# Optimization experiments

Measured on AMD Instinct MI355X. Metric: run time of the kernel, lower is better.

## Reference

```python
import jax, jax.numpy as jnp
import numpy as np

V = 32000; D = 512; H = 8; DH = D // H; L = 12; E = 8; FF = 2048
B = 2; S = 1024; MAXPOS = 2048
EPS = 1e-6; NEG = -1e9


def _rmsnorm(x, w):
    return x * jax.lax.rsqrt(jnp.mean(x * x, axis=-1, keepdims=True) + EPS) * w


def setup_inputs() -> dict:
    key = jax.random.key(0)
    ks = jax.random.split(key, 10)
    s = 0.02
    n = lambda k, shp: jax.random.normal(k, shp, jnp.float32) * s
    return {
        "input_ids": jax.random.randint(ks[0], (B, S), 0, V),
        "tok_emb": n(ks[1], (V, D)),
        "pos_emb": n(ks[2], (MAXPOS, D)),
        "Wqkv": n(ks[3], (L, D, 3 * D)), "bqkv": jnp.zeros((L, 3 * D), jnp.float32),
        "Wo": n(ks[4], (L, D, D)), "bo": jnp.zeros((L, D), jnp.float32),
        "rW": n(ks[5], (L, D, E)), "rb": jnp.zeros((L, E), jnp.float32),
        "eW1": n(ks[6], (L, E, D, FF)), "eb1": jnp.zeros((L, E, FF), jnp.float32),
        "eW2": n(ks[7], (L, E, FF, D)), "eb2": jnp.zeros((L, E, D), jnp.float32),
        "n1w": jnp.ones((L, D), jnp.float32), "n2w": jnp.ones((L, D), jnp.float32),
        "now": jnp.ones((D,), jnp.float32), "lmW": n(ks[8], (D, V)),
    }


def _forward(input_ids, tok_emb, pos_emb, Wqkv, bqkv, Wo, bo, rW, rb,
             eW1, eb1, eW2, eb2, n1w, n2w, now, lmW):
    x = tok_emb[input_ids] + pos_emb[:S]              # [B,S,D]
    causal = jnp.tril(jnp.ones((S, S), bool))         # lower-triangular mask

    def step(x, p):
        wqkv, bq, wo, bo_, rw, rb_, w1, b1, w2, b2, g1, g2 = p
        # --- causal self-attention ---
        h = _rmsnorm(x, g1)
        qkv = h @ wqkv + bq
        q, k, v = [t.reshape(B, S, H, DH) for t in jnp.split(qkv, 3, axis=-1)]
        scores = jnp.einsum('bqhd,bkhd->bhqk', q, k) / jnp.sqrt(jnp.float32(DH))
        scores = jnp.where(causal, scores, NEG)
        attn = jax.nn.softmax(scores, axis=-1)
        o = jnp.einsum('bhqk,bkhd->bqhd', attn, v).reshape(B, S, D) @ wo + bo_
        x = x + o
        # --- MoE layer, top-1 routing ---
        h = _rmsnorm(x, g2)
        rl = h @ rw + rb_                              # router logits [B,S,E]
        probs = jax.nn.softmax(rl, axis=-1)
        top_w = jnp.max(probs, axis=-1)                # top-1 gate weight [B,S]
        top_i = jnp.argmax(probs, axis=-1)             # expert id [B,S]
        one_hot = jax.nn.one_hot(top_i, E, dtype=x.dtype)
        frac = jnp.mean(one_hot, axis=(0, 1))          # fraction of tokens per expert
        pmean = jnp.mean(probs, axis=(0, 1))           # mean router prob per expert
        aux = E * jnp.sum(frac * pmean)                # switch-style load-balance loss
        disp = (one_hot * top_w[..., None]).reshape(-1, E)   # [T,E] weighted dispatch
        hf = h.reshape(-1, D)                          # [T,D]
        hid = jax.nn.gelu(jnp.einsum('td,edf->etf', hf, w1) + b1[:, None, :], approximate=False)
        outs = jnp.einsum('etf,efd->etd', hid, w2) + b2[:, None, :]
        y = jnp.einsum('etd,te->td', outs, disp).reshape(B, S, D)  # scatter-combine
        x = x + y
        return x, (aux, rl)

    x, (auxes, rlogits) = jax.lax.scan(
        step, x, (Wqkv, bqkv, Wo, bo, rW, rb, eW1, eb1, eW2, eb2, n1w, n2w))
    logits = _rmsnorm(x, now) @ lmW                    # [B,S,V]
    return logits, jnp.sum(auxes), rlogits


def reference(input_ids, tok_emb, pos_emb, Wqkv, bqkv, Wo, bo, rW, rb,
              eW1, eb1, eW2, eb2, n1w, n2w, now, lmW):
    return _forward(input_ids, tok_emb, pos_emb, Wqkv, bqkv, Wo, bo, rW, rb,
                    eW1, eb1, eW2, eb2, n1w, n2w, now, lmW)
```

## Files before the change

kernel.cpp:

```cpp
#include <hip/hip_runtime.h>

constexpr int B_  = 2, S_ = 1024, T_ = 2048;
constexpr int D_  = 512, H_ = 8, DH_ = 64;
constexpr int L_  = 12, E_ = 8, FF_ = 2048;
constexpr int V_  = 32000, D3_ = 1536;

using half8_t = __attribute__((ext_vector_type(8))) _Float16;
using half2_t = __attribute__((ext_vector_type(2))) _Float16;
using f32x4_t = __attribute__((ext_vector_type(4))) float;

__device__ __forceinline__ float wred(float v){
#pragma unroll
  for (int off = 32; off; off >>= 1) v += __shfl_xor(v, off);
  return v;
}
__device__ __forceinline__ float gelu_f(float v){
  return 0.5f * v * (1.f + erff(v * 0.70710678118654752f));
}

__global__ void k_embed(const int* __restrict__ ids, const float* __restrict__ tok,
                        const float* __restrict__ pos, float* __restrict__ x){
  int t = blockIdx.x;
  int s = t & (S_ - 1);
  int id = ids[t];
  const float* tr = tok + (size_t)id * D_;
  const float* pr = pos + (size_t)s  * D_;
  float* xr = x + (size_t)t * D_;
  for (int d = threadIdx.x; d < D_; d += blockDim.x) xr[d] = tr[d] + pr[d];
}

__global__ __launch_bounds__(64) void k_norm_router(
    const float* __restrict__ x, const float* __restrict__ nw,
    const float* __restrict__ rW, const float* __restrict__ rb,
    float* __restrict__ h, float* __restrict__ rl_out,
    float* __restrict__ topw, int* __restrict__ topi){
  const int t = blockIdx.x, lane = threadIdx.x;
  const float* xr = x + (size_t)t * D_;
  const float4 xv0 = *reinterpret_cast<const float4*>(xr + (lane << 2));
  const float4 xv1 = *reinterpret_cast<const float4*>(xr + 256 + (lane << 2));
  float ss = xv0.x*xv0.x + xv0.y*xv0.y + xv0.z*xv0.z + xv0.w*xv0.w
           + xv1.x*xv1.x + xv1.y*xv1.y + xv1.z*xv1.z + xv1.w*xv1.w;
  ss = wred(ss);
  const float sc = rsqrtf(ss * (1.f / (float)D_) + 1e-6f);
  const float4 w0 = *reinterpret_cast<const float4*>(nw + (lane << 2));
  const float4 w1 = *reinterpret_cast<const float4*>(nw + 256 + (lane << 2));
  float hv[8];
  hv[0] = xv0.x*sc*w0.x; hv[1] = xv0.y*sc*w0.y; hv[2] = xv0.z*sc*w0.z; hv[3] = xv0.w*sc*w0.w;
  hv[4] = xv1.x*sc*w1.x; hv[5] = xv1.y*sc*w1.y; hv[6] = xv1.z*sc*w1.z; hv[7] = xv1.w*sc*w1.w;
  float* hr = h + (size_t)t * D_;
  *reinterpret_cast<float4*>(hr + (lane << 2))       = make_float4(hv[0], hv[1], hv[2], hv[3]);
  *reinterpret_cast<float4*>(hr + 256 + (lane << 2)) = make_float4(hv[4], hv[5], hv[6], hv[7]);
  float acc[8] = {0,0,0,0,0,0,0,0};
#pragma unroll
  for (int u = 0; u < 8; u++){
    const int d = (u < 4) ? ((lane << 2) + u) : (256 + (lane << 2) + u - 4);
    const float4 ra = *reinterpret_cast<const float4*>(rW + (size_t)d * E_);
    const float4 rb4 = *reinterpret_cast<const float4*>(rW + (size_t)d * E_ + 4);
    acc[0] += hv[u]*ra.x;  acc[1] += hv[u]*ra.y;  acc[2] += hv[u]*ra.z;  acc[3] += hv[u]*ra.w;
    acc[4] += hv[u]*rb4.x; acc[5] += hv[u]*rb4.y; acc[6] += hv[u]*rb4.z; acc[7] += hv[u]*rb4.w;
  }
  float rl[8];
#pragma unroll
  for (int e = 0; e < 8; e++) rl[e] = wred(acc[e]) + rb[e];
  float mx = rl[0];
#pragma unroll
  for (int e = 1; e < 8; e++) mx = fmaxf(mx, rl[e]);
  float p[8], s = 0.f;
#pragma unroll
  for (int e = 0; e < 8; e++){ p[e] = __expf(rl[e] - mx); s += p[e]; }
  const float inv = 1.f / s;
  int arg = 0; float best = rl[0];
#pragma unroll
  for (int e = 1; e < 8; e++) if (rl[e] > best){ best = rl[e]; arg = e; }
  if (lane == 0){
#pragma unroll
    for (int e = 0; e < 8; e++) rl_out[(size_t)t * E_ + e] = rl[e];
    topw[t] = p[arg] * inv;
    topi[t] = arg;
  }
}

__global__ __launch_bounds__(1024) void k_route_scan2(
    const int* __restrict__ topi, const float* __restrict__ rl,
    int* __restrict__ seg, int* __restrict__ perm, float* __restrict__ aux){
  __shared__ int cnt[8], segs[9], cur[8];
  __shared__ float psums[8];
  const int tid = threadIdx.x;
  if (tid < 8){ cnt[tid] = 0; psums[tid] = 0.f; }
  __syncthreads();
  const int t0 = tid, t1 = tid + 1024;
  const int e0 = topi[t0], e1 = topi[t1];
  atomicAdd(&cnt[e0], 1);
  atomicAdd(&cnt[e1], 1);
  float ps[8] = {0,0,0,0,0,0,0,0};
#pragma unroll
  for (int k = 0; k < 2; k++){
    const float* r = rl + (size_t)(k ? t1 : t0) * E_;
    float v[8];
#pragma unroll
    for (int e = 0; e < 8; e++) v[e] = r[e];
    float mx = v[0];
#pragma unroll
    for (int e = 1; e < 8; e++) mx = fmaxf(mx, v[e]);
    float s = 0.f;
#pragma unroll
    for (int e = 0; e < 8; e++){ v[e] = __expf(v[e] - mx); s += v[e]; }
    const float is = 1.f / s;
#pragma unroll
    for (int e = 0; e < 8; e++) ps[e] += v[e] * is;
  }
#pragma unroll
  for (int e = 0; e < 8; e++) ps[e] = wred(ps[e]);
  if ((tid & 63) == 0){
#pragma unroll
    for (int e = 0; e < 8; e++) atomicAdd(&psums[e], ps[e]);
  }
  __syncthreads();
  if (tid == 0){
    segs[0] = 0;
#pragma unroll
    for (int e = 0; e < 8; e++) segs[e + 1] = segs[e] + cnt[e];
#pragma unroll
    for (int e = 0; e < 8; e++) cur[e] = segs[e];
  }
  __syncthreads();
  if (tid < 9) seg[tid] = segs[tid];
  const int p0 = atomicAdd(&cur[e0], 1); perm[p0] = t0;
  const int p1 = atomicAdd(&cur[e1], 1); perm[p1] = t1;
  if (tid == 0){
    float av = 0.f;
#pragma unroll
    for (int e = 0; e < 8; e++) av += (float)cnt[e] * psums[e];
    aux[0] += 8.f * av * (1.f / ((float)T_ * (float)T_));
  }
}

template<int BM, int BN, int NPROD, int EPI, bool MOE, bool APERM, int SWZROWS, bool ANORM>
__global__ __launch_bounds__(256) void k_mgemm(
    const float* __restrict__ A, const float* __restrict__ Bm,
    const float* __restrict__ bias, float* __restrict__ C,
    int M, int N, int K,
    const int* __restrict__ seg, const int* __restrict__ perm,
    const float* __restrict__ topw, const float* __restrict__ nw){
  constexpr int FM = BM / 32, FN = BN / 32;
  constexpr int BSLOTS = BN / 64;
  const int tid = threadIdx.x;
  int rowTile, colTile;
  if (SWZROWS > 0){
    const int nwg = gridDim.x;
    const int bid = blockIdx.x;
    const int lb = (bid & 7) * (nwg >> 3) + (bid >> 3);
    rowTile = lb % SWZROWS;
    colTile = lb / SWZROWS;
  } else {
    colTile = blockIdx.x; rowTile = blockIdx.y;
  }
  int e = 0, s0 = 0, cnt = M;
  if (MOE){ e = blockIdx.z; s0 = seg[e]; cnt = seg[e + 1] - s0; }
  const int row0 = rowTile * BM, col0 = colTile * BN;
  if (MOE && row0 >= cnt) return;
  const float* Bp = Bm + (size_t)e * K * N;
  const float* bp = bias + (size_t)e * N;

  __shared__ __align__(16) _Float16 Ah[BM * 32];
  __shared__ __align__(16) _Float16 Al[NPROD == 3 ? BM * 32 : 8];
  __shared__ __align__(16) _Float16 Bh[BN * 32];
  __shared__ __align__(16) _Float16 Bl[NPROD == 3 ? BN * 32 : 8];

  const int am = (BM == 64) ? (tid >> 2) : (tid >> 1);
  const int agrow = row0 + am;
  const bool aval = agrow < cnt;
  const float* Arow = nullptr;
  if (aval){
    int ridx = APERM ? perm[s0 + agrow] : (MOE ? s0 + agrow : agrow);
    Arow = A + (size_t)ridx * K;
  }
  const int asub = am >> 4;

  const int lane = tid & 63, w = tid >> 6;
  const int wm0 = (w >> 1) * (BM / 2), wn0 = (w & 1) * (BN / 2);

  float ascale = 1.f;
  if (ANORM){
    float ss = 0.f;
    if (BM == 64){
      const int kg = tid & 3;
      for (int k0 = 0; k0 < K; k0 += 32){
        const float4 a0 = *reinterpret_cast<const float4*>(Arow + k0 + (kg << 3));
        const float4 a1 = *reinterpret_cast<const float4*>(Arow + k0 + (kg << 3) + 4);
        ss += a0.x*a0.x + a0.y*a0.y + a0.z*a0.z + a0.w*a0.w
            + a1.x*a1.x + a1.y*a1.y + a1.z*a1.z + a1.w*a1.w;
      }
      ss += __shfl_xor(ss, 1);
      ss += __shfl_xor(ss, 2);
    } else {
      const int kgb = (tid & 1) << 1;
      for (int k0 = 0; k0 < K; k0 += 32){
#pragma unroll
        for (int kq = 0; kq < 2; kq++){
          const int kg = kgb + kq;
          const float4 a0 = *reinterpret_cast<const float4*>(Arow + k0 + (kg << 3));
          const float4 a1 = *reinterpret_cast<const float4*>(Arow + k0 + (kg << 3) + 4);
          ss += a0.x*a0.x + a0.y*a0.y + a0.z*a0.z + a0.w*a0.w
              + a1.x*a1.x + a1.y*a1.y + a1.z*a1.z + a1.w*a1.w;
        }
      }
      ss += __shfl_xor(ss, 1);
    }
    ascale = rsqrtf(ss * (1.f / (float)K) + 1e-6f);
  }

  f32x4_t acc_hh[FM][FN];
  f32x4_t acc_mx[NPROD == 3 ? FM : 1][NPROD == 3 ? FN : 1];
#pragma unroll
  for (int i = 0; i < FM; i++)
#pragma unroll
    for (int j = 0; j < FN; j++){
      acc_hh[i][j] = (f32x4_t){0.f, 0.f, 0.f, 0.f};
      if (NPROD == 3) acc_mx[i][j] = (f32x4_t){0.f, 0.f, 0.f, 0.f};
    }

  for (int k0 = 0; k0 < K; k0 += 32){
    if (BM == 64){
      const int kg = tid & 3;
      float4 av0 = make_float4(0,0,0,0), av1 = make_float4(0,0,0,0);
      if (aval){
        av0 = *reinterpret_cast<const float4*>(Arow + k0 + (kg << 3));
        av1 = *reinterpret_cast<const float4*>(Arow + k0 + (kg << 3) + 4);
      }
      float a8[8] = {av0.x, av0.y, av0.z, av0.w, av1.x, av1.y, av1.z, av1.w};
      if (ANORM){
        const float4 w0 = *reinterpret_cast<const float4*>(nw + k0 + (kg << 3));
        const float4 w1 = *reinterpret_cast<const float4*>(nw + k0 + (kg << 3) + 4);
        const float wn8[8] = {w0.x, w0.y, w0.z, w0.w, w1.x, w1.y, w1.z, w1.w};
#pragma unroll
        for (int u = 0; u < 8; u++) a8[u] *= ascale * wn8[u];
      }
      half8_t hi, lo;
#pragma unroll
      for (int u = 0; u < 8; u++){
        hi[u] = (_Float16)a8[u];
        if (NPROD == 3) lo[u] = (_Float16)((a8[u] - (float)hi[u]) * 2048.f);
      }
      const int lidx = (am & 15) + (kg << 4);
      const int base = asub * 512 + ((lidx ^ (asub & 7)) << 3);
      *reinterpret_cast<half8_t*>(&Ah[base]) = hi;
      if (NPROD == 3) *reinterpret_cast<half8_t*>(&Al[base]) = lo;
    } else {
      const int kgb = (tid & 1) << 1;
#pragma unroll
      for (int kq = 0; kq < 2; kq++){
        const int kg = kgb + kq;
        float4 av0 = make_float4(0,0,0,0), av1 = make_float4(0,0,0,0);
        if (aval){
          av0 = *reinterpret_cast<const float4*>(Arow + k0 + (kg << 3));
          av1 = *reinterpret_cast<const float4*>(Arow + k0 + (kg << 3) + 4);
        }
        float a8[8] = {av0.x, av0.y, av0.z, av0.w, av1.x, av1.y, av1.z, av1.w};
        if (ANORM){
          const float4 w0 = *reinterpret_cast<const float4*>(nw + k0 + (kg << 3));
          const float4 w1 = *reinterpret_cast<const float4*>(nw + k0 + (kg << 3) + 4);
          const float wn8[8] = {w0.x, w0.y, w0.z, w0.w, w1.x, w1.y, w1.z, w1.w};
#pragma unroll
          for (int u = 0; u < 8; u++) a8[u] *= ascale * wn8[u];
        }
        half8_t hi;
#pragma unroll
        for (int u = 0; u < 8; u++) hi[u] = (_Float16)a8[u];
        const int lidx = (am & 15) + (kg << 4);
        *reinterpret_cast<half8_t*>(&Ah[asub * 512 + ((lidx ^ (asub & 7)) << 3)]) = hi;
      }
    }
#pragma unroll
    for (int sl = 0; sl < BSLOTS; sl++){
      const int sid = sl * 256 + tid;
      const int col = sid & (BN - 1);
      const int kg  = sid / BN;
      const float* bpp = Bp + (size_t)(k0 + (kg << 3)) * N + col0 + col;
      half8_t hi, lo;
#pragma unroll
      for (int ee = 0; ee < 8; ee++){
        const float v = bpp[(size_t)ee * N];
        hi[ee] = (_Float16)v;
        if (NPROD == 3) lo[ee] = (_Float16)((v - (float)hi[ee]) * 2048.f);
      }
      const int sub = col >> 4;
      const int lidx = (col & 15) + (kg << 4);
      const int base = sub * 512 + ((lidx ^ (sub & 7)) << 3);
      *reinterpret_cast<half8_t*>(&Bh[base]) = hi;
      if (NPROD == 3) *reinterpret_cast<half8_t*>(&Bl[base]) = lo;
    }
    __syncthreads();
    half8_t fAh[FM], fBh[FN];
    half8_t fAl[NPROD == 3 ? FM : 1], fBl[NPROD == 3 ? FN : 1];
#pragma unroll
    for (int fm = 0; fm < FM; fm++){
      const int s = (wm0 >> 4) + fm;
      const int ofs = s * 512 + ((lane ^ (s & 7)) << 3);
      fAh[fm] = *reinterpret_cast<const half8_t*>(&Ah[ofs]);
      if (NPROD == 3) fAl[fm] = *reinterpret_cast<const half8_t*>(&Al[ofs]);
    }
#pragma unroll
    for (int fn = 0; fn < FN; fn++){
      const int s = (wn0 >> 4) + fn;
      const int ofs = s * 512 + ((lane ^ (s & 7)) << 3);
      fBh[fn] = *reinterpret_cast<const half8_t*>(&Bh[ofs]);
      if (NPROD == 3) fBl[fn] = *reinterpret_cast<const half8_t*>(&Bl[ofs]);
    }
#pragma unroll
    for (int fm = 0; fm < FM; fm++)
#pragma unroll
      for (int fn = 0; fn < FN; fn++){
        acc_hh[fm][fn] = __builtin_amdgcn_mfma_f32_16x16x32_f16(
            fAh[fm], fBh[fn], acc_hh[fm][fn], 0, 0, 0);
        if (NPROD == 3){
          acc_mx[fm][fn] = __builtin_amdgcn_mfma_f32_16x16x32_f16(
              fAh[fm], fBl[fn], acc_mx[fm][fn], 0, 0, 0);
          acc_mx[fm][fn] = __builtin_amdgcn_mfma_f32_16x16x32_f16(
              fAl[fm], fBh[fn], acc_mx[fm][fn], 0, 0, 0);
        }
      }
    __syncthreads();
  }

  const int lr = lane & 15, kg4 = lane >> 4;
#pragma unroll
  for (int fm = 0; fm < FM; fm++){
#pragma unroll
    for (int reg = 0; reg < 4; reg++){
      const int grow = row0 + wm0 + fm * 16 + (kg4 << 2) + reg;
      if (grow >= cnt) continue;
      int trow = 0; float tw = 0.f;
      if (EPI == 3){ trow = perm[s0 + grow]; tw = topw[trow]; }
#pragma unroll
      for (int fn = 0; fn < FN; fn++){
        const int col = col0 + wn0 + fn * 16 + lr;
        float v = acc_hh[fm][fn][reg];
        if (NPROD == 3) v += acc_mx[fm][fn][reg] * (1.f / 2048.f);
        if (EPI == 0){
          C[(size_t)grow * N + col] = v + bp[col];
        } else if (EPI == 1){
          C[(size_t)grow * N + col] += v + bp[col];
        } else if (EPI == 2){
          C[(size_t)(s0 + grow) * N + col] = gelu_f(v + bp[col]);
        } else if (EPI == 3){
          C[(size_t)trow * N + col] += tw * (v + bp[col]);
        } else {
          C[(size_t)grow * N + col] = v;
        }
      }
    }
  }
}

__global__ __launch_bounds__(256) void k_attn5(const float* __restrict__ qkv,
                                               float* __restrict__ o,
                                               float* __restrict__ attp,
                                               float* __restrict__ attml){
  __shared__ __align__(16) _Float16 Khi[4096], Klo[4096], Vhi[4096], Vlo[4096];
  __shared__ __align__(16) float pbuf[4][16 * 68];
  const int tid = threadIdx.x, w = tid >> 6, lane = tid & 63;
  const int lr = lane & 15, g = lane >> 4;
  const int bid = blockIdx.x;
  int bh, qt, kt0, kt1, mode;
  if (bid < 128){        bh = bid >> 3;            qt = 8 + (bid & 7);  kt0 = 0; kt1 = 7;  mode = 1; }
  else if (bid < 256){   const int j = bid - 128;  bh = j >> 3; qt = 7 - (j & 7);  kt0 = 0; kt1 = qt; mode = 0; }
  else {                 const int j = bid - 256;  bh = j >> 3; qt = 15 - (j & 7); kt0 = 8; kt1 = qt; mode = 2; }
  const int b = bh >> 3, h = bh & 7;
  const size_t bbase = (size_t)(b << 10) * D3_;
  const int hoff = h * 64;
  const int qg = (qt << 6) + (w << 4) + lr;

  half8_t qhi[2], qlo[2];
#pragma unroll
  for (int ks = 0; ks < 2; ks++){
    const float* qp = qkv + bbase + (size_t)qg * D3_ + hoff + ks * 32 + g * 8;
    const float4 f0 = *reinterpret_cast<const float4*>(qp);
    const float4 f1 = *reinterpret_cast<const float4*>(qp + 4);
    const float qa[8] = {f0.x, f0.y, f0.z, f0.w, f1.x, f1.y, f1.z, f1.w};
#pragma unroll
    for (int e = 0; e < 8; e++){
      const float v = qa[e] * 0.125f;
      const _Float16 hi = (_Float16)v;
      qhi[ks][e] = hi;
      qlo[ks][e] = (_Float16)((v - (float)hi) * 2048.f);
    }
  }

  float m = -1e30f, l = 0.f;
  f32x4_t oacc[4];
#pragma unroll
  for (int s = 0; s < 4; s++) oacc[s] = (f32x4_t){0.f, 0.f, 0.f, 0.f};

  const int kK = tid >> 2, quad = tid & 3;
  const int kp = tid >> 3, oct = tid & 7;

  float ka[16], va[8], vb[8];
  auto loadregs = [&](int kt){
    const int j0 = kt << 6;
    const float* kr = qkv + bbase + (size_t)(j0 + kK) * D3_ + 512 + hoff + quad * 16;
    const float4 f0 = *reinterpret_cast<const float4*>(kr);
    const float4 f1 = *reinterpret_cast<const float4*>(kr + 4);
    const float4 f2 = *reinterpret_cast<const float4*>(kr + 8);
    const float4 f3 = *reinterpret_cast<const float4*>(kr + 12);
    ka[0]=f0.x; ka[1]=f0.y; ka[2]=f0.z; ka[3]=f0.w;
    ka[4]=f1.x; ka[5]=f1.y; ka[6]=f1.z; ka[7]=f1.w;
    ka[8]=f2.x; ka[9]=f2.y; ka[10]=f2.z; ka[11]=f2.w;
    ka[12]=f3.x; ka[13]=f3.y; ka[14]=f3.z; ka[15]=f3.w;
    const int k0v = kp << 1;
    const float* vr = qkv + bbase + (size_t)(j0 + k0v) * D3_ + 1024 + hoff + oct * 8;
    const float4 a0 = *reinterpret_cast<const float4*>(vr);
    const float4 a1 = *reinterpret_cast<const float4*>(vr + 4);
    const float4 b0 = *reinterpret_cast<const float4*>(vr + D3_);
    const float4 b1 = *reinterpret_cast<const float4*>(vr + D3_ + 4);
    va[0]=a0.x; va[1]=a0.y; va[2]=a0.z; va[3]=a0.w;
    va[4]=a1.x; va[5]=a1.y; va[6]=a1.z; va[7]=a1.w;
    vb[0]=b0.x; vb[1]=b0.y; vb[2]=b0.z; vb[3]=b0.w;
    vb[4]=b1.x; vb[5]=b1.y; vb[6]=b1.z; vb[7]=b1.w;
  };
  auto writelds = [&](){
    const int ksd = quad >> 1;
#pragma unroll
    for (int ch = 0; ch < 2; ch++){
      const int kgd = ((quad << 1) + ch) & 3;
      const int base = ksd * 2048 + (kK >> 4) * 512 + (((kK & 15) + (kgd << 4)) << 3);
      half8_t hi, lo;
#pragma unroll
      for (int e = 0; e < 8; e++){
        const float v = ka[ch * 8 + e];
        const _Float16 hv = (_Float16)v;
        hi[e] = hv;
        lo[e] = (_Float16)((v - (float)hv) * 2048.f);
      }
      *reinterpret_cast<half8_t*>(&Khi[base]) = hi;
      *reinterpret_cast<half8_t*>(&Klo[base]) = lo;
    }
    const int ksk = kp >> 4, kgk = (kp >> 2) & 3, e0 = (kp & 3) << 1;
#pragma unroll
    for (int j = 0; j < 8; j++){
      const int d = oct * 8 + j;
      const int lidx = (d & 15) + (kgk << 4);
      const int sw = lidx ^ kgk ^ (ksk << 2);
      const int fa = ksk * 2048 + (d >> 4) * 512 + (sw << 3) + e0;
      const _Float16 h0 = (_Float16)va[j], h1 = (_Float16)vb[j];
      *reinterpret_cast<half2_t*>(&Vhi[fa]) = (half2_t){h0, h1};
      const _Float16 l0 = (_Float16)((va[j] - (float)h0) * 2048.f);
      const _Float16 l1 = (_Float16)((vb[j] - (float)h1) * 2048.f);
      *reinterpret_cast<half2_t*>(&Vlo[fa]) = (half2_t){l0, l1};
    }
  };

  loadregs(kt0);
  for (int kt = kt0; kt <= kt1; kt++){
    const int j0 = kt << 6;
    __syncthreads();
    writelds();
    if (kt < kt1) loadregs(kt + 1);
    __syncthreads();

    f32x4_t dfr[4];
#pragma unroll
    for (int s = 0; s < 4; s++){
      f32x4_t acc = (f32x4_t){0.f, 0.f, 0.f, 0.f};
      f32x4_t mix = (f32x4_t){0.f, 0.f, 0.f, 0.f};
#pragma unroll
      for (int ks = 0; ks < 2; ks++){
        const int base = ks * 2048 + s * 512 + lane * 8;
        const half8_t khi = *reinterpret_cast<const half8_t*>(&Khi[base]);
        const half8_t klo = *reinterpret_cast<const half8_t*>(&Klo[base]);
        acc = __builtin_amdgcn_mfma_f32_16x16x32_f16(khi, qhi[ks], acc, 0, 0, 0);
        mix = __builtin_amdgcn_mfma_f32_16x16x32_f16(khi, qlo[ks], mix, 0, 0, 0);
        mix = __builtin_amdgcn_mfma_f32_16x16x32_f16(klo, qhi[ks], mix, 0, 0, 0);
      }
#pragma unroll
      for (int r = 0; r < 4; r++) dfr[s][r] = acc[r] + mix[r] * (1.f / 2048.f);
    }
    if (kt == qt){
#pragma unroll
      for (int s = 0; s < 4; s++)
#pragma unroll
        for (int r = 0; r < 4; r++){
          const int keyg = j0 + (g << 2) + r + (s << 4);
          if (keyg > qg) dfr[s][r] = -1e30f;
        }
    }
    float mloc = dfr[0][0];
#pragma unroll
    for (int s = 0; s < 4; s++)
#pragma unroll
      for (int r = 0; r < 4; r++) mloc = fmaxf(mloc, dfr[s][r]);
    mloc = fmaxf(mloc, __shfl_xor(mloc, 16));
    mloc = fmaxf(mloc, __shfl_xor(mloc, 32));
    const float mn = fmaxf(m, mloc);
    const float cr = __expf(m - mn);
    float psum = 0.f;
#pragma unroll
    for (int s = 0; s < 4; s++)
#pragma unroll
      for (int r = 0; r < 4; r++){
        const float p = __expf(dfr[s][r] - mn);
        psum += p;
        pbuf[w][lr * 68 + (s << 4) + (g << 2) + r] = p;
      }
    psum += __shfl_xor(psum, 16);
    psum += __shfl_xor(psum, 32);
    l = l * cr + psum;
    m = mn;
#pragma unroll
    for (int s = 0; s < 4; s++)
#pragma unroll
      for (int r = 0; r < 4; r++) oacc[s][r] *= cr;

    half8_t phi[2], plo[2];
#pragma unroll
    for (int ks = 0; ks < 2; ks++){
      const float* pp = &pbuf[w][lr * 68 + ks * 32 + g * 8];
      const float4 p0 = *reinterpret_cast<const float4*>(pp);
      const float4 p1 = *reinterpret_cast<const float4*>(pp + 4);
      const float pa[8] = {p0.x,p0.y,p0.z,p0.w, p1.x,p1.y,p1.z,p1.w};
#pragma unroll
      for (int e = 0; e < 8; e++){
        const _Float16 hv = (_Float16)pa[e];
        phi[ks][e] = hv;
        plo[ks][e] = (_Float16)((pa[e] - (float)hv) * 2048.f);
      }
    }
#pragma unroll
    for (int s = 0; s < 4; s++){
      f32x4_t mix = (f32x4_t){0.f, 0.f, 0.f, 0.f};
#pragma unroll
      for (int ks = 0; ks < 2; ks++){
        const int sw = lane ^ g ^ (ks << 2);
        const int base = ks * 2048 + s * 512 + sw * 8;
        const half8_t vhi = *reinterpret_cast<const half8_t*>(&Vhi[base]);
        const half8_t vlo = *reinterpret_cast<const half8_t*>(&Vlo[base]);
        oacc[s] = __builtin_amdgcn_mfma_f32_16x16x32_f16(vhi, phi[ks], oacc[s], 0, 0, 0);
        mix = __builtin_amdgcn_mfma_f32_16x16x32_f16(vhi, plo[ks], mix, 0, 0, 0);
        mix = __builtin_amdgcn_mfma_f32_16x16x32_f16(vlo, phi[ks], mix, 0, 0, 0);
      }
#pragma unroll
      for (int r = 0; r < 4; r++) oacc[s][r] += mix[r] * (1.f / 2048.f);
    }
  }

  if (mode == 0){
    const float linv = 1.f / l;
    float* orow = o + (size_t)((b << 10) + qg) * D_ + hoff;
#pragma unroll
    for (int s = 0; s < 4; s++)
#pragma unroll
      for (int r = 0; r < 4; r++){
        const int d = (g << 2) + r + (s << 4);
        orow[d] = oacc[s][r] * linv;
      }
  } else {
    const int pidx = (((bh << 3) + (qt - 8)) << 1) + (mode - 1);
    float* pO = attp + (size_t)pidx * 4096;
    const int qloc = (w << 4) + lr;
#pragma unroll
    for (int s = 0; s < 4; s++)
#pragma unroll
      for (int r = 0; r < 4; r++){
        const int d = (g << 2) + r + (s << 4);
        pO[qloc * 64 + d] = oacc[s][r];
      }
    if (g == 0){
      attml[pidx * 128 + qloc]      = m;
      attml[pidx * 128 + 64 + qloc] = l;
    }
  }
}

__global__ __launch_bounds__(256) void k_attn_comb(const float* __restrict__ attp,
                                                   const float* __restrict__ attml,
                                                   float* __restrict__ o){
  const int bid = blockIdx.x;
  const int bh = bid >> 3, i = bid & 7, qt = 8 + i;
  const int b = bh >> 3, h = bh & 7;
  const int pidx0 = ((bh << 3) + i) << 1;
  const float* pA = attp + (size_t)pidx0 * 4096;
  const float* pB = pA + 4096;
  const float* mlA = attml + pidx0 * 128;
  const float* mlB = mlA + 128;
  const int tid = threadIdx.x;
  const int q = tid >> 2, dg = (tid & 3) << 4;
  const float mA = mlA[q], lA = mlA[64 + q];
  const float mB = mlB[q], lB = mlB[64 + q];
  const float M = fmaxf(mA, mB);
  const float cA = __expf(mA - M), cB = __expf(mB - M);
  const float linv = 1.f / (lA * cA + lB * cB);
  float* orow = o + (size_t)((b << 10) + (qt << 6) + q) * D_ + h * 64;
#pragma unroll
  for (int j = 0; j < 4; j++){
    const int d = dg + (j << 2);
    const float4 a = *reinterpret_cast<const float4*>(pA + q * 64 + d);
    const float4 bb = *reinterpret_cast<const float4*>(pB + q * 64 + d);
    *reinterpret_cast<float4*>(orow + d) = make_float4(
        (a.x * cA + bb.x * cB) * linv, (a.y * cA + bb.y * cB) * linv,
        (a.z * cA + bb.z * cB) * linv, (a.w * cA + bb.w * cB) * linv);
  }
}

extern "C" void kernel_launch(void* const* d_in, const int* in_sizes, int n_in,
                              void* d_out, int out_size, void* d_ws, size_t ws_size,
                              hipStream_t stream){
  const int*   ids  = (const int*)  d_in[0];
  const float* tok  = (const float*)d_in[1];
  const float* pos  = (const float*)d_in[2];
  const float* Wqkv = (const float*)d_in[3];
  const float* bqkv = (const float*)d_in[4];
  const float* Wo   = (const float*)d_in[5];
  const float* bo   = (const float*)d_in[6];
  const float* rW   = (const float*)d_in[7];
  const float* rb   = (const float*)d_in[8];
  const float* eW1  = (const float*)d_in[9];
  const float* eb1  = (const float*)d_in[10];
  const float* eW2  = (const float*)d_in[11];
  const float* eb2  = (const float*)d_in[12];
  const float* n1w  = (const float*)d_in[13];
  const float* n2w  = (const float*)d_in[14];
  const float* noww = (const float*)d_in[15];
  const float* lmW  = (const float*)d_in[16];

  float* out    = (float*)d_out;
  float* logits = out;
  float* aux    = out + (size_t)T_ * V_;
  float* rlog   = aux + 1;

  float* ws = (float*)d_ws;
  size_t off = 0;
  float* x     = ws + off; off += (size_t)T_ * D_;
  float* h     = ws + off; off += (size_t)T_ * D_;
  float* qkv   = ws + off; off += (size_t)T_ * D3_;
  float* attno = ws + off; off += (size_t)T_ * D_;
  float* hid   = ws + off; off += (size_t)T_ * FF_;
  float* topw  = ws + off; off += T_;
  int* topi    = (int*)(ws + off); off += T_;
  int* perm    = (int*)(ws + off); off += T_;
  int* seg     = (int*)(ws + off); off += (E_ + 1);
  float* attp  = ws + off; off += 16 * 8 * 2 * 4096;
  float* attml = ws + off; off += 16 * 8 * 2 * 128;

  hipMemsetAsync(aux, 0, sizeof(float), stream);
  k_embed<<<T_, 256, 0, stream>>>(ids, tok, pos, x);

  for (int l = 0; l < L_; l++){
    k_mgemm<64, 128, 3, 0, false, false, 0, true><<<dim3(D3_ / 128, T_ / 64), 256, 0, stream>>>(
        x, Wqkv + (size_t)l * D_ * D3_, bqkv + (size_t)l * D3_, qkv,
        T_, D3_, D_, seg, perm, topw, n1w + (size_t)l * D_);
    k_attn5<<<384, 256, 0, stream>>>(qkv, attno, attp, attml);
    k_attn_comb<<<128, 256, 0, stream>>>(attp, attml, attno);
    k_mgemm<64, 64, 3, 1, false, false, 0, false><<<dim3(D_ / 64, T_ / 64), 256, 0, stream>>>(
        attno, Wo + (size_t)l * D_ * D_, bo + (size_t)l * D_, x,
        T_, D_, D_, seg, perm, topw, nullptr);
    k_norm_router<<<T_, 64, 0, stream>>>(x, n2w + (size_t)l * D_,
        rW + (size_t)l * D_ * E_, rb + (size_t)l * E_,
        h, rlog + (size_t)l * T_ * E_, topw, topi);
    k_route_scan2<<<1, 1024, 0, stream>>>(topi, rlog + (size_t)l * T_ * E_, seg, perm, aux);
    k_mgemm<64, 128, 3, 2, true, true, 0, false><<<dim3(FF_ / 128, T_ / 64, E_), 256, 0, stream>>>(
        h, eW1 + (size_t)l * E_ * D_ * FF_, eb1 + (size_t)l * E_ * FF_, hid,
        T_, FF_, D_, seg, perm, topw, nullptr);
    k_mgemm<64, 64, 3, 3, true, false, 0, false><<<dim3(D_ / 64, T_ / 64, E_), 256, 0, stream>>>(
        hid, eW2 + (size_t)l * E_ * FF_ * D_, eb2 + (size_t)l * E_ * D_, x,
        T_, D_, FF_, seg, perm, topw, nullptr);
  }

  k_mgemm<128, 128, 1, 4, false, false, 16, true><<<(T_ / 128) * (V_ / 128), 256, 0, stream>>>(
      x, lmW, nullptr, logits, T_, V_, D_, seg, perm, topw, noww);
}
```

Measured before the change: 3.214 ms.

## Prefetch next K-tile into registers and pre-pack LM head weights to fp16

The GEMM main loop now loads the next K-step's A and B tiles into registers before the MFMA work on the current tile, then writes them to shared memory after the barrier. This is register-level software pipelining meant to hide global-load latency behind compute. A new prep kernel converts the LM-head weight matrix to fp16 in the exact swizzled tile layout, so the vocab GEMM can do contiguous half8 copies instead of strided fp32 loads plus conversion. The packed weights reuse the qkv/attno/hid workspace. The costs are an extra full pass over lmW on every call and higher register pressure from the prefetch buffers.

```diff
diff --git a/kernel.cpp b/kernel.cpp
--- a/kernel.cpp
+++ b/kernel.cpp
@@ -135,13 +135,29 @@
   }
 }
 
-template<int BM, int BN, int NPROD, int EPI, bool MOE, bool APERM, int SWZROWS, bool ANORM>
+__global__ __launch_bounds__(256) void k_prep_lm(const float* __restrict__ Bsrc,
+                                                 _Float16* __restrict__ Bpre){
+  const int gid = blockIdx.x * 256 + threadIdx.x;
+  const int n = gid % V_;
+  const int kb = gid / V_;
+  const int kstep = kb >> 2, kg = kb & 3;
+  const int colTile = n >> 7, nl = n & 127;
+  const int sub = nl >> 4;
+  const int lsw = ((nl & 15) + (kg << 4)) ^ (sub & 7);
+  half8_t v;
+#pragma unroll
+  for (int e = 0; e < 8; e++) v[e] = (_Float16)Bsrc[(size_t)(kb * 8 + e) * V_ + n];
+  *reinterpret_cast<half8_t*>(&Bpre[(((size_t)colTile * 16 + kstep) << 12) + sub * 512 + lsw * 8]) = v;
+}
+
+template<int BM, int BN, int NPROD, int EPI, bool MOE, bool APERM, int SWZROWS, bool ANORM, bool BPRE>
 __global__ __launch_bounds__(256) void k_mgemm(
     const float* __restrict__ A, const float* __restrict__ Bm,
     const float* __restrict__ bias, float* __restrict__ C,
     int M, int N, int K,
     const int* __restrict__ seg, const int* __restrict__ perm,
-    const float* __restrict__ topw, const float* __restrict__ nw){
+    const float* __restrict__ topw, const float* __restrict__ nw,
+    const _Float16* __restrict__ Bpre){
   constexpr int FM = BM / 32, FN = BN / 32;
   constexpr int BSLOTS = BN / 64;
   const int tid = threadIdx.x;
@@ -210,25 +226,54 @@
     ascale = rsqrtf(ss * (1.f / (float)K) + 1e-6f);
   }
 
-  f32x4_t acc_hh[FM][FN];
-  f32x4_t acc_mx[NPROD == 3 ? FM : 1][NPROD == 3 ? FN : 1];
-#pragma unroll
-  for (int i = 0; i < FM; i++)
-#pragma unroll
-    for (int j = 0; j < FN; j++){
-      acc_hh[i][j] = (f32x4_t){0.f, 0.f, 0.f, 0.f};
-      if (NPROD == 3) acc_mx[i][j] = (f32x4_t){0.f, 0.f, 0.f, 0.f};
-    }
-
-  for (int k0 = 0; k0 < K; k0 += 32){
-    if (BM == 64){
-      const int kg = tid & 3;
-      float4 av0 = make_float4(0,0,0,0), av1 = make_float4(0,0,0,0);
+  float areg[(BM == 64) ? 8 : 1];
+  float breg[BPRE ? 1 : BSLOTS * 8];
+  half8_t bh8[BPRE ? 2 : 1];
+
+  auto aload64 = [&](int k0){
+    const int kg = tid & 3;
+    float4 a0 = make_float4(0,0,0,0), a1 = make_float4(0,0,0,0);
+    if (aval){
+      a0 = *reinterpret_cast<const float4*>(Arow + k0 + (kg << 3));
+      a1 = *reinterpret_cast<const float4*>(Arow + k0 + (kg << 3) + 4);
+    }
+    areg[0]=a0.x; areg[1]=a0.y; areg[2]=a0.z; areg[3]=a0.w;
+    areg[4]=a1.x; areg[5]=a1.y; areg[6]=a1.z; areg[7]=a1.w;
+  };
+  auto astore64 = [&](int k0){
+    const int kg = tid & 3;
+    float a8[8];
+#pragma unroll
+    for (int u = 0; u < 8; u++) a8[u] = areg[u];
+    if (ANORM){
+      const float4 w0 = *reinterpret_cast<const float4*>(nw + k0 + (kg << 3));
+      const float4 w1 = *reinterpret_cast<const float4*>(nw + k0 + (kg << 3) + 4);
+      const float wn8[8] = {w0.x, w0.y, w0.z, w0.w, w1.x, w1.y, w1.z, w1.w};
+#pragma unroll
+      for (int u = 0; u < 8; u++) a8[u] *= ascale * wn8[u];
+    }
+    half8_t hi, lo;
+#pragma unroll
+    for (int u = 0; u < 8; u++){
+      hi[u] = (_Float16)a8[u];
+      if (NPROD == 3) lo[u] = (_Float16)((a8[u] - (float)hi[u]) * 2048.f);
+    }
+    const int lidx = (am & 15) + (kg << 4);
+    const int base = asub * 512 + ((lidx ^ (asub & 7)) << 3);
+    *reinterpret_cast<half8_t*>(&Ah[base]) = hi;
+    if (NPROD == 3) *reinterpret_cast<half8_t*>(&Al[base]) = lo;
+  };
+  auto astore128 = [&](int k0){
+    const int kgb = (tid & 1) << 1;
+#pragma unroll
+    for (int kq = 0; kq < 2; kq++){
+      const int kg = kgb + kq;
+      float4 a0 = make_float4(0,0,0,0), a1 = make_float4(0,0,0,0);
       if (aval){
-        av0 = *reinterpret_cast<const float4*>(Arow + k0 + (kg << 3));
-        av1 = *reinterpret_cast<const float4*>(Arow + k0 + (kg << 3) + 4);
-      }
-      float a8[8] = {av0.x, av0.y, av0.z, av0.w, av1.x, av1.y, av1.z, av1.w};
+        a0 = *reinterpret_cast<const float4*>(Arow + k0 + (kg << 3));
+        a1 = *reinterpret_cast<const float4*>(Arow + k0 + (kg << 3) + 4);
+      }
+      float a8[8] = {a0.x, a0.y, a0.z, a0.w, a1.x, a1.y, a1.z, a1.w};
       if (ANORM){
         const float4 w0 = *reinterpret_cast<const float4*>(nw + k0 + (kg << 3));
         const float4 w1 = *reinterpret_cast<const float4*>(nw + k0 + (kg << 3) + 4);
@@ -236,61 +281,80 @@
 #pragma unroll
         for (int u = 0; u < 8; u++) a8[u] *= ascale * wn8[u];
       }
-      half8_t hi, lo;
-#pragma unroll
-      for (int u = 0; u < 8; u++){
-        hi[u] = (_Float16)a8[u];
-        if (NPROD == 3) lo[u] = (_Float16)((a8[u] - (float)hi[u]) * 2048.f);
-      }
+      half8_t hi;
+#pragma unroll
+      for (int u = 0; u < 8; u++) hi[u] = (_Float16)a8[u];
       const int lidx = (am & 15) + (kg << 4);
-      const int base = asub * 512 + ((lidx ^ (asub & 7)) << 3);
-      *reinterpret_cast<half8_t*>(&Ah[base]) = hi;
-      if (NPROD == 3) *reinterpret_cast<half8_t*>(&Al[base]) = lo;
+      *reinterpret_cast<half8_t*>(&Ah[asub * 512 + ((lidx ^ (asub & 7)) << 3)]) = hi;
+    }
+  };
+  auto bload = [&](int k0){
+    if (BPRE){
+      const _Float16* bsrc = Bpre + (((size_t)colTile * 16 + (k0 >> 5)) << 12);
+#pragma unroll
+      for (int r = 0; r < 2; r++)
+        bh8[r] = *reinterpret_cast<const half8_t*>(&bsrc[(r * 256 + tid) * 8]);
     } else {
-      const int kgb = (tid & 1) << 1;
-#pragma unroll
-      for (int kq = 0; kq < 2; kq++){
-        const int kg = kgb + kq;
-        float4 av0 = make_float4(0,0,0,0), av1 = make_float4(0,0,0,0);
-        if (aval){
-          av0 = *reinterpret_cast<const float4*>(Arow + k0 + (kg << 3));
-          av1 = *reinterpret_cast<const float4*>(Arow + k0 + (kg << 3) + 4);
+#pragma unroll
+      for (int sl = 0; sl < BSLOTS; sl++){
+        const int sid = sl * 256 + tid;
+        const int col = sid & (BN - 1);
+        const int kg  = sid / BN;
+        const float* bpp = Bp + (size_t)(k0 + (kg << 3)) * N + col0 + col;
+#pragma unroll
+        for (int ee = 0; ee < 8; ee++) breg[sl * 8 + ee] = bpp[(size_t)ee * N];
+      }
+    }
+  };
+  auto bstore = [&](){
+    if (BPRE){
+#pragma unroll
+      for (int r = 0; r < 2; r++)
+        *reinterpret_cast<half8_t*>(&Bh[(r * 256 + tid) * 8]) = bh8[r];
+    } else {
+#pragma unroll
+      for (int sl = 0; sl < BSLOTS; sl++){
+        const int sid = sl * 256 + tid;
+        const int col = sid & (BN - 1);
+        const int kg  = sid / BN;
+        half8_t hi, lo;
+#pragma unroll
+        for (int ee = 0; ee < 8; ee++){
+          const float v = breg[sl * 8 + ee];
+          hi[ee] = (_Float16)v;
+          if (NPROD == 3) lo[ee] = (_Float16)((v - (float)hi[ee]) * 2048.f);
         }
-        float a8[8] = {av0.x, av0.y, av0.z, av0.w, av1.x, av1.y, av1.z, av1.w};
-        if (ANORM){
-          const float4 w0 = *reinterpret_cast<const float4*>(nw + k0 + (kg << 3));
-          const float4 w1 = *reinterpret_cast<const float4*>(nw + k0 + (kg << 3) + 4);
-          const float wn8[8] = {w0.x, w0.y, w0.z, w0.w, w1.x, w1.y, w1.z, w1.w};
-#pragma unroll
-          for (int u = 0; u < 8; u++) a8[u] *= ascale * wn8[u];
-        }
-        half8_t hi;
-#pragma unroll
-        for (int u = 0; u < 8; u++) hi[u] = (_Float16)a8[u];
-        const int lidx = (am & 15) + (kg << 4);
-        *reinterpret_cast<half8_t*>(&Ah[asub * 512 + ((lidx ^ (asub & 7)) << 3)]) = hi;
-      }
-    }
-#pragma unroll
-    for (int sl = 0; sl < BSLOTS; sl++){
-      const int sid = sl * 256 + tid;
-      const int col = sid & (BN - 1);
-      const int kg  = sid / BN;
-      const float* bpp = Bp + (size_t)(k0 + (kg << 3)) * N + col0 + col;
-      half8_t hi, lo;
-#pragma unroll
-      for (int ee = 0; ee < 8; ee++){
-        const float v = bpp[(size_t)ee * N];
-        hi[ee] = (_Float16)v;
-        if (NPROD == 3) lo[ee] = (_Float16)((v - (float)hi[ee]) * 2048.f);
-      }
-      const int sub = col >> 4;
-      const int lidx = (col & 15) + (kg << 4);
-      const int base = sub * 512 + ((lidx ^ (sub & 7)) << 3);
-      *reinterpret_cast<half8_t*>(&Bh[base]) = hi;
-      if (NPROD == 3) *reinterpret_cast<half8_t*>(&Bl[base]) = lo;
-    }
-    __syncthreads();
+        const int sub = col >> 4;
+        const int lidx = (col & 15) + (kg << 4);
+        const int base = sub * 512 + ((lidx ^ (sub & 7)) << 3);
+        *reinterpret_cast<half8_t*>(&Bh[base]) = hi;
+        if (NPROD == 3) *reinterpret_cast<half8_t*>(&Bl[base]) = lo;
+      }
+    }
+  };
+
+  f32x4_t acc_hh[FM][FN];
+  f32x4_t acc_mx[NPROD == 3 ? FM : 1][NPROD == 3 ? FN : 1];
+#pragma unroll
+  for (int i = 0; i < FM; i++)
+#pragma unroll
+    for (int j = 0; j < FN; j++){
+      acc_hh[i][j] = (f32x4_t){0.f, 0.f, 0.f, 0.f};
+      if (NPROD == 3) acc_mx[i][j] = (f32x4_t){0.f, 0.f, 0.f, 0.f};
+    }
+
+  if (BM == 64) aload64(0);
+  bload(0);
+  if (BM == 64) astore64(0); else astore128(0);
+  bstore();
+  __syncthreads();
+
+  for (int k0 = 0; k0 < K; k0 += 32){
+    const bool hasNext = (k0 + 32 < K);
+    if (hasNext){
+      if (BM == 64) aload64(k0 + 32);
+      bload(k0 + 32);
+    }
     half8_t fAh[FM], fBh[FN];
     half8_t fAl[NPROD == 3 ? FM : 1], fBl[NPROD == 3 ? FN : 1];
 #pragma unroll
@@ -321,6 +385,11 @@
         }
       }
     __syncthreads();
+    if (hasNext){
+      if (BM == 64) astore64(k0 + 32); else astore128(k0 + 32);
+      bstore();
+      __syncthreads();
+    }
   }
 
   const int lr = lane & 15, kg4 = lane >> 4;
@@ -645,26 +714,28 @@
   k_embed<<<T_, 256, 0, stream>>>(ids, tok, pos, x);
 
   for (int l = 0; l < L_; l++){
-    k_mgemm<64, 128, 3, 0, false, false, 0, true><<<dim3(D3_ / 128, T_ / 64), 256, 0, stream>>>(
+    k_mgemm<64, 128, 3, 0, false, false, 0, true, false><<<dim3(D3_ / 128, T_ / 64), 256, 0, stream>>>(
         x, Wqkv + (size_t)l * D_ * D3_, bqkv + (size_t)l * D3_, qkv,
-        T_, D3_, D_, seg, perm, topw, n1w + (size_t)l * D_);
+        T_, D3_, D_, seg, perm, topw, n1w + (size_t)l * D_, nullptr);
     k_attn5<<<384, 256, 0, stream>>>(qkv, attno, attp, attml);
     k_attn_comb<<<128, 256, 0, stream>>>(attp, attml, attno);
-    k_mgemm<64, 64, 3, 1, false, false, 0, false><<<dim3(D_ / 64, T_ / 64), 256, 0, stream>>>(
+    k_mgemm<64, 64, 3, 1, false, false, 0, false, false><<<dim3(D_ / 64, T_ / 64), 256, 0, stream>>>(
         attno, Wo + (size_t)l * D_ * D_, bo + (size_t)l * D_, x,
-        T_, D_, D_, seg, perm, topw, nullptr);
+        T_, D_, D_, seg, perm, topw, nullptr, nullptr);
     k_norm_router<<<T_, 64, 0, stream>>>(x, n2w + (size_t)l * D_,
         rW + (size_t)l * D_ * E_, rb + (size_t)l * E_,
         h, rlog + (size_t)l * T_ * E_, topw, topi);
     k_route_scan2<<<1, 1024, 0, stream>>>(topi, rlog + (size_t)l * T_ * E_, seg, perm, aux);
-    k_mgemm<64, 128, 3, 2, true, true, 0, false><<<dim3(FF_ / 128, T_ / 64, E_), 256, 0, stream>>>(
+    k_mgemm<64, 128, 3, 2, true, true, 0, false, false><<<dim3(FF_ / 128, T_ / 64, E_), 256, 0, stream>>>(
         h, eW1 + (size_t)l * E_ * D_ * FF_, eb1 + (size_t)l * E_ * FF_, hid,
-        T_, FF_, D_, seg, perm, topw, nullptr);
-    k_mgemm<64, 64, 3, 3, true, false, 0, false><<<dim3(D_ / 64, T_ / 64, E_), 256, 0, stream>>>(
+        T_, FF_, D_, seg, perm, topw, nullptr, nullptr);
+    k_mgemm<64, 64, 3, 3, true, false, 0, false, false><<<dim3(D_ / 64, T_ / 64, E_), 256, 0, stream>>>(
         hid, eW2 + (size_t)l * E_ * FF_ * D_, eb2 + (size_t)l * E_ * D_, x,
-        T_, D_, FF_, seg, perm, topw, nullptr);
-  }
-
-  k_mgemm<128, 128, 1, 4, false, false, 16, true><<<(T_ / 128) * (V_ / 128), 256, 0, stream>>>(
-      x, lmW, nullptr, logits, T_, V_, D_, seg, perm, topw, noww);
-}
+        T_, D_, FF_, seg, perm, topw, nullptr, nullptr);
+  }
+
+  _Float16* lmw16 = (_Float16*)qkv;
+  k_prep_lm<<<(64 * V_) / 256, 256, 0, stream>>>(lmW, lmw16);
+  k_mgemm<128, 128, 1, 4, false, false, 16, true, true><<<(T_ / 128) * (V_ / 128), 256, 0, stream>>>(
+      x, lmW, nullptr, logits, T_, V_, D_, seg, perm, topw, noww, lmw16);
+}
```

After: 3.468 ms. +7.9%, slower.

## Prepack LM-head weights to fp16 swizzled tiles and deepen GEMM K-step

Applied to the files above, without the earlier changes.

Adds a pre-pass that converts the LM-head weight matrix into fp16 tiles already laid out in the swizzled shared-memory order, so the LM GEMM copies them with vector loads instead of doing strided fp32 loads and conversions. The scratch area for these tiles starts at the QKV workspace and extends into the idle buffers after it. It also doubles the per-iteration K depth of all GEMMs to 64, halving barrier count per tile at the cost of twice the shared memory, which may reduce occupancy for the split-precision variants.

```diff
diff --git a/kernel.cpp b/kernel.cpp
--- a/kernel.cpp
+++ b/kernel.cpp
@@ -135,15 +135,34 @@
   }
 }
 
-template<int BM, int BN, int NPROD, int EPI, bool MOE, bool APERM, int SWZROWS, bool ANORM>
+__global__ __launch_bounds__(256) void k_prep_lm(const float* __restrict__ Bsrc,
+                                                 _Float16* __restrict__ Bpre){
+  const int gid = blockIdx.x * 256 + threadIdx.x;
+  const int n = gid % V_;
+  const int kb = gid / V_;
+  const int kstep = kb >> 3, kgl = kb & 7;
+  const int ks2 = kgl >> 2, kg = kgl & 3;
+  const int colTile = n >> 7, nl = n & 127;
+  const int sub = nl >> 4;
+  const int lsw = ((nl & 15) + (kg << 4)) ^ (sub & 7);
+  half8_t v;
+#pragma unroll
+  for (int e = 0; e < 8; e++) v[e] = (_Float16)Bsrc[(size_t)(kb * 8 + e) * V_ + n];
+  *reinterpret_cast<half8_t*>(
+      &Bpre[((size_t)(colTile * 8 + kstep) << 13) + ks2 * 4096 + sub * 512 + lsw * 8]) = v;
+}
+
+template<int BM, int BN, int NPROD, int EPI, bool MOE, bool APERM, int SWZROWS, bool ANORM, bool BPRE>
 __global__ __launch_bounds__(256) void k_mgemm(
     const float* __restrict__ A, const float* __restrict__ Bm,
     const float* __restrict__ bias, float* __restrict__ C,
     int M, int N, int K,
     const int* __restrict__ seg, const int* __restrict__ perm,
-    const float* __restrict__ topw, const float* __restrict__ nw){
+    const float* __restrict__ topw, const float* __restrict__ nw,
+    const _Float16* __restrict__ Bpre){
   constexpr int FM = BM / 32, FN = BN / 32;
-  constexpr int BSLOTS = BN / 64;
+  constexpr int AKS = BM * 32, BKS = BN * 32;
+  constexpr int BSLOTS = BN / 32;
   const int tid = threadIdx.x;
   int rowTile, colTile;
   if (SWZROWS > 0){
@@ -162,10 +181,10 @@
   const float* Bp = Bm + (size_t)e * K * N;
   const float* bp = bias + (size_t)e * N;
 
-  __shared__ __align__(16) _Float16 Ah[BM * 32];
-  __shared__ __align__(16) _Float16 Al[NPROD == 3 ? BM * 32 : 8];
-  __shared__ __align__(16) _Float16 Bh[BN * 32];
-  __shared__ __align__(16) _Float16 Bl[NPROD == 3 ? BN * 32 : 8];
+  __shared__ __align__(16) _Float16 Ah[BM * 64];
+  __shared__ __align__(16) _Float16 Al[NPROD == 3 ? BM * 64 : 8];
+  __shared__ __align__(16) _Float16 Bh[BN * 64];
+  __shared__ __align__(16) _Float16 Bl[NPROD == 3 ? BN * 64 : 8];
 
   const int am = (BM == 64) ? (tid >> 2) : (tid >> 1);
   const int agrow = row0 + am;
@@ -220,106 +239,103 @@
       if (NPROD == 3) acc_mx[i][j] = (f32x4_t){0.f, 0.f, 0.f, 0.f};
     }
 
-  for (int k0 = 0; k0 < K; k0 += 32){
-    if (BM == 64){
-      const int kg = tid & 3;
-      float4 av0 = make_float4(0,0,0,0), av1 = make_float4(0,0,0,0);
-      if (aval){
-        av0 = *reinterpret_cast<const float4*>(Arow + k0 + (kg << 3));
-        av1 = *reinterpret_cast<const float4*>(Arow + k0 + (kg << 3) + 4);
-      }
-      float a8[8] = {av0.x, av0.y, av0.z, av0.w, av1.x, av1.y, av1.z, av1.w};
-      if (ANORM){
-        const float4 w0 = *reinterpret_cast<const float4*>(nw + k0 + (kg << 3));
-        const float4 w1 = *reinterpret_cast<const float4*>(nw + k0 + (kg << 3) + 4);
-        const float wn8[8] = {w0.x, w0.y, w0.z, w0.w, w1.x, w1.y, w1.z, w1.w};
-#pragma unroll
-        for (int u = 0; u < 8; u++) a8[u] *= ascale * wn8[u];
-      }
-      half8_t hi, lo;
-#pragma unroll
-      for (int u = 0; u < 8; u++){
-        hi[u] = (_Float16)a8[u];
-        if (NPROD == 3) lo[u] = (_Float16)((a8[u] - (float)hi[u]) * 2048.f);
-      }
-      const int lidx = (am & 15) + (kg << 4);
-      const int base = asub * 512 + ((lidx ^ (asub & 7)) << 3);
-      *reinterpret_cast<half8_t*>(&Ah[base]) = hi;
-      if (NPROD == 3) *reinterpret_cast<half8_t*>(&Al[base]) = lo;
+  for (int k0 = 0; k0 < K; k0 += 64){
+    {
+      constexpr int NCH = (BM == 64) ? 2 : 4;
+      const int kq = (BM == 64) ? (tid & 3) : (tid & 1);
+#pragma unroll
+      for (int c = 0; c < NCH; c++){
+        const int kgt = kq * NCH + c;
+        const int k = k0 + (kgt << 3);
+        float4 a0 = make_float4(0,0,0,0), a1 = make_float4(0,0,0,0);
+        if (aval){
+          a0 = *reinterpret_cast<const float4*>(Arow + k);
+          a1 = *reinterpret_cast<const float4*>(Arow + k + 4);
+        }
+        float a8[8] = {a0.x, a0.y, a0.z, a0.w, a1.x, a1.y, a1.z, a1.w};
+        if (ANORM){
+          const float4 w0 = *reinterpret_cast<const float4*>(nw + k);
+          const float4 w1 = *reinterpret_cast<const float4*>(nw + k + 4);
+          const float wn8[8] = {w0.x, w0.y, w0.z, w0.w, w1.x, w1.y, w1.z, w1.w};
+#pragma unroll
+          for (int u = 0; u < 8; u++) a8[u] *= ascale * wn8[u];
+        }
+        half8_t hi, lo;
+#pragma unroll
+        for (int u = 0; u < 8; u++){
+          hi[u] = (_Float16)a8[u];
+          if (NPROD == 3) lo[u] = (_Float16)((a8[u] - (float)hi[u]) * 2048.f);
+        }
+        const int ks2 = kgt >> 2, kg = kgt & 3;
+        const int lidx = (am & 15) + (kg << 4);
+        const int base = ks2 * AKS + asub * 512 + ((lidx ^ (asub & 7)) << 3);
+        *reinterpret_cast<half8_t*>(&Ah[base]) = hi;
+        if (NPROD == 3) *reinterpret_cast<half8_t*>(&Al[base]) = lo;
+      }
+    }
+    if (BPRE){
+      const _Float16* bsrc = Bpre + (((size_t)colTile * (K >> 6) + (k0 >> 6)) << 13);
+#pragma unroll
+      for (int r = 0; r < 4; r++){
+        const int ofs = (r * 256 + tid) * 8;
+        *reinterpret_cast<half8_t*>(&Bh[ofs]) =
+            *reinterpret_cast<const half8_t*>(&bsrc[ofs]);
+      }
     } else {
-      const int kgb = (tid & 1) << 1;
-#pragma unroll
-      for (int kq = 0; kq < 2; kq++){
-        const int kg = kgb + kq;
-        float4 av0 = make_float4(0,0,0,0), av1 = make_float4(0,0,0,0);
-        if (aval){
-          av0 = *reinterpret_cast<const float4*>(Arow + k0 + (kg << 3));
-          av1 = *reinterpret_cast<const float4*>(Arow + k0 + (kg << 3) + 4);
-        }
-        float a8[8] = {av0.x, av0.y, av0.z, av0.w, av1.x, av1.y, av1.z, av1.w};
-        if (ANORM){
-          const float4 w0 = *reinterpret_cast<const float4*>(nw + k0 + (kg << 3));
-          const float4 w1 = *reinterpret_cast<const float4*>(nw + k0 + (kg << 3) + 4);
-          const float wn8[8] = {w0.x, w0.y, w0.z, w0.w, w1.x, w1.y, w1.z, w1.w};
-#pragma unroll
-          for (int u = 0; u < 8; u++) a8[u] *= ascale * wn8[u];
-        }
-        half8_t hi;
-#pragma unroll
-        for (int u = 0; u < 8; u++) hi[u] = (_Float16)a8[u];
-        const int lidx = (am & 15) + (kg << 4);
-        *reinterpret_cast<half8_t*>(&Ah[asub * 512 + ((lidx ^ (asub & 7)) << 3)]) = hi;
-      }
-    }
-#pragma unroll
-    for (int sl = 0; sl < BSLOTS; sl++){
-      const int sid = sl * 256 + tid;
-      const int col = sid & (BN - 1);
-      const int kg  = sid / BN;
-      const float* bpp = Bp + (size_t)(k0 + (kg << 3)) * N + col0 + col;
-      half8_t hi, lo;
-#pragma unroll
-      for (int ee = 0; ee < 8; ee++){
-        const float v = bpp[(size_t)ee * N];
-        hi[ee] = (_Float16)v;
-        if (NPROD == 3) lo[ee] = (_Float16)((v - (float)hi[ee]) * 2048.f);
-      }
-      const int sub = col >> 4;
-      const int lidx = (col & 15) + (kg << 4);
-      const int base = sub * 512 + ((lidx ^ (sub & 7)) << 3);
-      *reinterpret_cast<half8_t*>(&Bh[base]) = hi;
-      if (NPROD == 3) *reinterpret_cast<half8_t*>(&Bl[base]) = lo;
+#pragma unroll
+      for (int sl = 0; sl < BSLOTS; sl++){
+        const int sid = sl * 256 + tid;
+        const int col = sid & (BN - 1);
+        const int kgt = sid / BN;
+        const float* bpp = Bp + (size_t)(k0 + (kgt << 3)) * N + col0 + col;
+        half8_t hi, lo;
+#pragma unroll
+        for (int ee = 0; ee < 8; ee++){
+          const float v = bpp[(size_t)ee * N];
+          hi[ee] = (_Float16)v;
+          if (NPROD == 3) lo[ee] = (_Float16)((v - (float)hi[ee]) * 2048.f);
+        }
+        const int ks2 = kgt >> 2, kg = kgt & 3;
+        const int sub = col >> 4;
+        const int lidx = (col & 15) + (kg << 4);
+        const int base = ks2 * BKS + sub * 512 + ((lidx ^ (sub & 7)) << 3);
+        *reinterpret_cast<half8_t*>(&Bh[base]) = hi;
+        if (NPROD == 3) *reinterpret_cast<half8_t*>(&Bl[base]) = lo;
+      }
     }
     __syncthreads();
-    half8_t fAh[FM], fBh[FN];
-    half8_t fAl[NPROD == 3 ? FM : 1], fBl[NPROD == 3 ? FN : 1];
-#pragma unroll
-    for (int fm = 0; fm < FM; fm++){
-      const int s = (wm0 >> 4) + fm;
-      const int ofs = s * 512 + ((lane ^ (s & 7)) << 3);
-      fAh[fm] = *reinterpret_cast<const half8_t*>(&Ah[ofs]);
-      if (NPROD == 3) fAl[fm] = *reinterpret_cast<const half8_t*>(&Al[ofs]);
-    }
-#pragma unroll
-    for (int fn = 0; fn < FN; fn++){
-      const int s = (wn0 >> 4) + fn;
-      const int ofs = s * 512 + ((lane ^ (s & 7)) << 3);
-      fBh[fn] = *reinterpret_cast<const half8_t*>(&Bh[ofs]);
-      if (NPROD == 3) fBl[fn] = *reinterpret_cast<const half8_t*>(&Bl[ofs]);
-    }
-#pragma unroll
-    for (int fm = 0; fm < FM; fm++)
+#pragma unroll
+    for (int ks2 = 0; ks2 < 2; ks2++){
+      half8_t fAh[FM], fBh[FN];
+      half8_t fAl[NPROD == 3 ? FM : 1], fBl[NPROD == 3 ? FN : 1];
+#pragma unroll
+      for (int fm = 0; fm < FM; fm++){
+        const int s = (wm0 >> 4) + fm;
+        const int ofs = ks2 * AKS + s * 512 + ((lane ^ (s & 7)) << 3);
+        fAh[fm] = *reinterpret_cast<const half8_t*>(&Ah[ofs]);
+        if (NPROD == 3) fAl[fm] = *reinterpret_cast<const half8_t*>(&Al[ofs]);
+      }
 #pragma unroll
       for (int fn = 0; fn < FN; fn++){
-        acc_hh[fm][fn] = __builtin_amdgcn_mfma_f32_16x16x32_f16(
-            fAh[fm], fBh[fn], acc_hh[fm][fn], 0, 0, 0);
-        if (NPROD == 3){
-          acc_mx[fm][fn] = __builtin_amdgcn_mfma_f32_16x16x32_f16(
-              fAh[fm], fBl[fn], acc_mx[fm][fn], 0, 0, 0);
-          acc_mx[fm][fn] = __builtin_amdgcn_mfma_f32_16x16x32_f16(
-              fAl[fm], fBh[fn], acc_mx[fm][fn], 0, 0, 0);
-        }
-      }
+        const int s = (wn0 >> 4) + fn;
+        const int ofs = ks2 * BKS + s * 512 + ((lane ^ (s & 7)) << 3);
+        fBh[fn] = *reinterpret_cast<const half8_t*>(&Bh[ofs]);
+        if (NPROD == 3) fBl[fn] = *reinterpret_cast<const half8_t*>(&Bl[ofs]);
+      }
+#pragma unroll
+      for (int fm = 0; fm < FM; fm++)
+#pragma unroll
+        for (int fn = 0; fn < FN; fn++){
+          acc_hh[fm][fn] = __builtin_amdgcn_mfma_f32_16x16x32_f16(
+              fAh[fm], fBh[fn], acc_hh[fm][fn], 0, 0, 0);
+          if (NPROD == 3){
+            acc_mx[fm][fn] = __builtin_amdgcn_mfma_f32_16x16x32_f16(
+                fAh[fm], fBl[fn], acc_mx[fm][fn], 0, 0, 0);
+            acc_mx[fm][fn] = __builtin_amdgcn_mfma_f32_16x16x32_f16(
+                fAl[fm], fBh[fn], acc_mx[fm][fn], 0, 0, 0);
+          }
+        }
+    }
     __syncthreads();
   }
 
@@ -645,26 +661,28 @@
   k_embed<<<T_, 256, 0, stream>>>(ids, tok, pos, x);
 
   for (int l = 0; l < L_; l++){
-    k_mgemm<64, 128, 3, 0, false, false, 0, true><<<dim3(D3_ / 128, T_ / 64), 256, 0, stream>>>(
+    k_mgemm<64, 128, 3, 0, false, false, 0, true, false><<<dim3(D3_ / 128, T_ / 64), 256, 0, stream>>>(
         x, Wqkv + (size_t)l * D_ * D3_, bqkv + (size_t)l * D3_, qkv,
-        T_, D3_, D_, seg, perm, topw, n1w + (size_t)l * D_);
+        T_, D3_, D_, seg, perm, topw, n1w + (size_t)l * D_, nullptr);
     k_attn5<<<384, 256, 0, stream>>>(qkv, attno, attp, attml);
     k_attn_comb<<<128, 256, 0, stream>>>(attp, attml, attno);
-    k_mgemm<64, 64, 3, 1, false, false, 0, false><<<dim3(D_ / 64, T_ / 64), 256, 0, stream>>>(
+    k_mgemm<64, 64, 3, 1, false, false, 0, false, false><<<dim3(D_ / 64, T_ / 64), 256, 0, stream>>>(
         attno, Wo + (size_t)l * D_ * D_, bo + (size_t)l * D_, x,
-        T_, D_, D_, seg, perm, topw, nullptr);
+        T_, D_, D_, seg, perm, topw, nullptr, nullptr);
     k_norm_router<<<T_, 64, 0, stream>>>(x, n2w + (size_t)l * D_,
         rW + (size_t)l * D_ * E_, rb + (size_t)l * E_,
         h, rlog + (size_t)l * T_ * E_, topw, topi);
     k_route_scan2<<<1, 1024, 0, stream>>>(topi, rlog + (size_t)l * T_ * E_, seg, perm, aux);
-    k_mgemm<64, 128, 3, 2, true, true, 0, false><<<dim3(FF_ / 128, T_ / 64, E_), 256, 0, stream>>>(
+    k_mgemm<64, 128, 3, 2, true, true, 0, false, false><<<dim3(FF_ / 128, T_ / 64, E_), 256, 0, stream>>>(
         h, eW1 + (size_t)l * E_ * D_ * FF_, eb1 + (size_t)l * E_ * FF_, hid,
-        T_, FF_, D_, seg, perm, topw, nullptr);
-    k_mgemm<64, 64, 3, 3, true, false, 0, false><<<dim3(D_ / 64, T_ / 64, E_), 256, 0, stream>>>(
+        T_, FF_, D_, seg, perm, topw, nullptr, nullptr);
+    k_mgemm<64, 64, 3, 3, true, false, 0, false, false><<<dim3(D_ / 64, T_ / 64, E_), 256, 0, stream>>>(
         hid, eW2 + (size_t)l * E_ * FF_ * D_, eb2 + (size_t)l * E_ * D_, x,
-        T_, D_, FF_, seg, perm, topw, nullptr);
-  }
-
-  k_mgemm<128, 128, 1, 4, false, false, 16, true><<<(T_ / 128) * (V_ / 128), 256, 0, stream>>>(
-      x, lmW, nullptr, logits, T_, V_, D_, seg, perm, topw, noww);
-}
+        T_, D_, FF_, seg, perm, topw, nullptr, nullptr);
+  }
+
+  _Float16* lmw16 = (_Float16*)qkv;
+  k_prep_lm<<<(64 * V_) / 256, 256, 0, stream>>>(lmW, lmw16);
+  k_mgemm<128, 128, 1, 4, false, false, 16, true, true><<<(T_ / 128) * (V_ / 128), 256, 0, stream>>>(
+      x, lmW, nullptr, logits, T_, V_, D_, seg, perm, topw, noww, lmw16);
+}
```

Result: no change. 3.197 ms, median of 2 (-0.5%).
